# Kernel optimization log

Hardware: AMD Instinct MI355X
Metric: run time of the kernel (lower is better)

The kernel has to match this reference:

```python
import jax, jax.numpy as jnp
import numpy as np
from jax import lax

B, BANDS, H, W = 128, 100, 9, 9
S = 10  # BANDS = S*S spectral grid
C_HID, OUT_CH = 16, 10
K = 3  # 3x3x3x3 kernel, SAME padding
DN = ('NCEFGH', 'OIEFGH', 'NCEFGH')  # 4 spatial dims E,F,G,H


def _conv4d(x, w, b):
    # x: [B, Cin, S, S, H, W], w: [Cout, Cin, 3, 3, 3, 3]
    y = lax.conv_general_dilated(x, w, (1, 1, 1, 1), 'SAME', dimension_numbers=DN)
    return y + b[None, :, None, None, None, None]


def setup_inputs() -> dict:
    key = jax.random.key(0)
    ks = jax.random.split(key, 13)
    x = jax.random.normal(ks[0], (B, BANDS, H, W), dtype=jnp.float32)
    p = {}
    cin = 1
    for i in range(5):
        p[f'w{i+1}'] = jax.random.normal(ks[1 + 2 * i], (C_HID, cin, K, K, K, K), dtype=jnp.float32) * 0.1
        p[f'b{i+1}'] = jax.random.normal(ks[2 + 2 * i], (C_HID,), dtype=jnp.float32) * 0.1
        cin = C_HID
    p['fc_w'] = jax.random.normal(ks[11], (OUT_CH, C_HID), dtype=jnp.float32) * 0.1
    p['fc_b'] = jax.random.normal(ks[12], (OUT_CH,), dtype=jnp.float32) * 0.1
    return {'x': x, **p}


def reference(x, w1, b1, w2, b2, w3, b3, w4, b4, w5, b5, fc_w, fc_b):
    b, c, h, w = x.shape
    # center_pixel: spectral difference w.r.t. the center pixel
    ctr = x[:, :, h // 2, w // 2]                 # [B, bands]
    local = x - ctr[:, :, None, None]             # [B, bands, H, W]
    # compute_local_feature: fold spectral axis into a 2D grid -> 6D, 1 channel
    pt = local.reshape(b, 1, S, S, h, w)          # [B, 1, S, S, H, W]
    a = pt
    for wgt, bia in ((w1, b1), (w2, b2), (w3, b3), (w4, b4), (w5, b5)):
        a = jax.nn.relu(_conv4d(a, wgt, bia))
    # sideout2d: pool spectral dims, per-pixel MLP readout
    feat = a.mean(axis=(2, 3))                    # [B, 16, H, W]
    out = jnp.einsum('bchw,oc->bohw', feat, fc_w) + fc_b[None, :, None, None]
    return out
```

## Files before the change

kernel.cpp:

```cpp
#include <hip/hip_runtime.h>

#define BB 128
#define CH 16
#define NBANDS 100
#define OUTC 10

#define P1PLANE 121
#define P1POS   17424

#define PFPLANE 132
#define PFPOS   19008

#define LPLANE  4224
#define NPLANES 16
#define LDSTILE (NPLANES*LPLANE + 768)
#define NCHUNK  (NPLANES*132)
#define NKP     5
#define WPL4    (NKP*9*64)

typedef unsigned short ushort_t;
typedef unsigned int uint_t;
typedef __attribute__((ext_vector_type(8))) short short8;
typedef __attribute__((ext_vector_type(4))) float f32x4;

__device__ __forceinline__ ushort_t f2bf(float f) {
    unsigned u = __float_as_uint(f);
    unsigned r = u + 0x7fffu + ((u >> 16) & 1u);
    return (ushort_t)(r >> 16);
}
__device__ __forceinline__ uint_t pk2(float a, float b) {
    return (uint_t)f2bf(a) | ((uint_t)f2bf(b) << 16);
}
__device__ __forceinline__ int swz(int x) { return x ^ ((x >> 3) & 0x30); }

template<int CTRL>
__device__ __forceinline__ short8 dpp_shift(short8 v) {
    union { short8 s; int i[4]; } a, b;
    a.s = v;
    #pragma unroll
    for (int k = 0; k < 4; ++k)
        b.i[k] = __builtin_amdgcn_update_dpp(0, a.i[k], CTRL, 0xf, 0xf, true);
    return b.s;
}

__global__ void prep_kernel(const float* __restrict__ x, float* __restrict__ bufP, int nb) {
    int idx = blockIdx.x * 256 + threadIdx.x;
    if (idx >= nb * PFPOS) return;
    int pos = idx % PFPOS;
    int b = idx / PFPOS;
    int e = pos / 1584;
    int r = pos % 1584;
    int f = r / 132;
    int s = r % 132;
    int g = s / 12, h = s % 12;
    float v = 0.f;
    if (e >= 1 && e <= 10 && f >= 1 && f <= 10 && g >= 1 && g <= 9 && h >= 1 && h <= 9) {
        const float* xp = x + ((size_t)b * NBANDS + (e - 1) * 10 + (f - 1)) * 81;
        v = xp[(g - 1) * 9 + (h - 1)] - xp[40];
    }
    bufP[idx] = v;
}

__global__ void pack_w_kernel(const float* __restrict__ w2, const float* __restrict__ w3,
                              const float* __restrict__ w4, const float* __restrict__ w5,
                              uint4* __restrict__ wp) {
    int t = blockIdx.x * 256 + threadIdx.x;
    if (t >= WPL4) return;
    int layer = blockIdx.y;
    const float* w = (layer == 0) ? w2 : (layer == 1) ? w3 : (layer == 2) ? w4 : w5;
    int l = t & 63, pd = t >> 6;
    int kp = pd / 9, q = pd % 9;
    int co = l & 15, kh = l >> 4;
    int m = kh >> 1, cih = (kh & 1) * 8;
    int c = 2 * kp + m;
    uint_t r[4] = {0, 0, 0, 0};
    if (c <= 8) {
        int tap = c * 9 + q;
        #pragma unroll
        for (int jj = 0; jj < 4; ++jj) {
            ushort_t lo = f2bf(w[(co * 16 + cih + 2 * jj) * 81 + tap]);
            ushort_t hi = f2bf(w[(co * 16 + cih + 2 * jj + 1) * 81 + tap]);
            r[jj] = (uint_t)lo | ((uint_t)hi << 16);
        }
    }
    uint4 v; v.x = r[0]; v.y = r[1]; v.z = r[2]; v.w = r[3];
    wp[(size_t)layer * WPL4 + t] = v;
}

__global__ __launch_bounds__(256) void conv1_kernel(
    const float* __restrict__ in, const float* __restrict__ w,
    const float* __restrict__ bias, ushort_t* __restrict__ out) {
    int idx = blockIdx.x * 256 + threadIdx.x;
    if (idx >= 900) return;
    int b = blockIdx.z;
    int co0 = blockIdx.y * 8;
    int g = idx % 9;
    int f = (idx / 9) % 10;
    int e = idx / 90;

    float acc[8][9];
    #pragma unroll
    for (int co = 0; co < 8; ++co) {
        float bv = bias[co0 + co];
        #pragma unroll
        for (int h = 0; h < 9; ++h) acc[co][h] = bv;
    }

    const float* ip = in + (size_t)b * PFPOS;
    #pragma unroll
    for (int de = 0; de < 3; ++de)
    #pragma unroll
    for (int df = 0; df < 3; ++df)
    #pragma unroll
    for (int dg = 0; dg < 3; ++dg) {
        const float4* rp4 = (const float4*)(ip + ((e + de) * 12 + (f + df)) * PFPLANE + (g + dg) * 12);
        float4 r0 = rp4[0], r1 = rp4[1], r2 = rp4[2];
        float v[12] = {r0.x, r0.y, r0.z, r0.w, r1.x, r1.y, r1.z, r1.w, r2.x, r2.y, r2.z, r2.w};
        #pragma unroll
        for (int dh = 0; dh < 3; ++dh) {
            int tap = de * 27 + df * 9 + dg * 3 + dh;
            #pragma unroll
            for (int co = 0; co < 8; ++co) {
                float ws = w[(co0 + co) * 81 + tap];
                #pragma unroll
                for (int h = 0; h < 9; ++h)
                    acc[co][h] = fmaf(ws, v[h + dh], acc[co][h]);
            }
        }
    }

    ushort_t* op = out + ((size_t)b * P1POS + ((e + 1) * 12 + (f + 1)) * P1PLANE + (g + 1) * 11 + 1) * 16 + co0;
    #pragma unroll
    for (int h = 0; h < 9; ++h) {
        uint4 q;
        q.x = pk2(fmaxf(acc[0][h], 0.f), fmaxf(acc[1][h], 0.f));
        q.y = pk2(fmaxf(acc[2][h], 0.f), fmaxf(acc[3][h], 0.f));
        q.z = pk2(fmaxf(acc[4][h], 0.f), fmaxf(acc[5][h], 0.f));
        q.w = pk2(fmaxf(acc[6][h], 0.f), fmaxf(acc[7][h], 0.f));
        *(uint4*)(op + h * 16) = q;
    }
}

__device__ __forceinline__ void stage_chunk(const ushort_t* __restrict__ gin,
                                            char* __restrict__ sIn, int i, int eb, int fb) {
    int h = i % 12;
    int gp = i / 12;
    int g = gp % 11;
    int pl = gp / 11;
    int pe = pl >> 2, pf = pl & 3;
    int e2 = eb + pe, f2 = fb + pf;
    bool valid = (e2 >= 1) & (e2 <= 10) & (f2 >= 1) & (f2 <= 10) &
                 (g >= 1) & (g <= 9) & (h >= 1) & (h <= 9);
    uint4 q0 = make_uint4(0, 0, 0, 0), q1 = q0;
    if (valid) {
        const uint4* g4 = (const uint4*)(gin + (size_t)((e2 * 12 + f2) * P1PLANE + g * 11 + h) * 16);
        q0 = g4[0]; q1 = g4[1];
    }
    *(uint4*)(sIn + swz(i * 32))      = q0;
    *(uint4*)(sIn + swz(i * 32 + 16)) = q1;
}

template<int GO0, int NT, int GI0, int GI1>
__device__ __forceinline__ void conv_col(
    const char* __restrict__ sIn, const short8* __restrict__ wv8, int l, int we, int wf,
    float bv, int e_out, int f_out, ushort_t* __restrict__ gout) {

    int h = l & 15, kh = l >> 4;
    int m = kh >> 1;
    int half16 = (kh & 1) * 16;
    int co = l & 15;

    f32x4 acc[NT];
    #pragma unroll
    for (int t = 0; t < NT; ++t) acc[t] = f32x4{bv, bv, bv, bv};

    #pragma unroll 1
    for (int kp = 0; kp < NKP; ++kp) {
        int c = 2 * kp + m; if (c > 8) c = 8;
        int pl = (we + c / 3) * 4 + (wf + c % 3);
        int pbase = pl * LPLANE + h * 32 + half16;

        short8 Bf[9];
        #pragma unroll
        for (int q = 0; q < 9; ++q) Bf[q] = wv8[(kp * 9 + q) * 64 + l];

        #pragma unroll
        for (int gi = GI0; gi <= GI1; ++gi) {
            short8 a1 = *(const short8*)(sIn + swz(pbase + gi * 384));
            short8 a0 = dpp_shift<0x111>(a1);
            short8 a2 = dpp_shift<0x101>(a1);
            #pragma unroll
            for (int dg = 0; dg < 3; ++dg) {
                int go = gi + 1 - dg;
                if (go >= GO0 && go < GO0 + NT) {
                    int t = go - GO0;
                    acc[t] = __builtin_amdgcn_mfma_f32_16x16x32_bf16(a0, Bf[dg * 3 + 0], acc[t], 0, 0, 0);
                    acc[t] = __builtin_amdgcn_mfma_f32_16x16x32_bf16(a1, Bf[dg * 3 + 1], acc[t], 0, 0, 0);
                    acc[t] = __builtin_amdgcn_mfma_f32_16x16x32_bf16(a2, Bf[dg * 3 + 2], acc[t], 0, 0, 0);
                }
            }
        }
    }

    #pragma unroll
    for (int t = 0; t < NT; ++t) {
        int go = GO0 + t;
        int base = ((e_out * 12 + f_out) * P1PLANE + go * 11) * 16 + co;
        #pragma unroll
        for (int reg = 0; reg < 4; ++reg) {
            int rr = kh * 4 + reg;
            if (rr >= 1 && rr <= 9)
                gout[base + rr * 16] = f2bf(fmaxf(acc[t][reg], 0.f));
        }
    }
}

__global__ __launch_bounds__(512, 4) void conv_mfma_kernel(
    const ushort_t* __restrict__ in, const uint4* __restrict__ wp,
    const float* __restrict__ bias, ushort_t* __restrict__ out) {

    __shared__ __align__(16) char sIn[LDSTILE];

    int tid = threadIdx.x;
    int b  = blockIdx.y;
    int eb = (blockIdx.x / 5) * 2;
    int fb = (blockIdx.x % 5) * 2;

    const ushort_t* gin = in + (size_t)b * P1POS * 16;
    #pragma unroll
    for (int k = 0; k < 4; ++k)
        stage_chunk(gin, sIn, tid + k * 512, eb, fb);
    if (tid < 64)
        stage_chunk(gin, sIn, tid + 2048, eb, fb);
    __syncthreads();

    int l = tid & 63, wv = tid >> 6;
    int col = wv >> 1, gs = wv & 1;
    int we = col >> 1, wf = col & 1;
    int e_out = eb + 1 + we;
    int f_out = fb + 1 + wf;
    float bv = bias[l & 15];

    ushort_t* gout = out + (size_t)b * P1POS * 16;
    const short8* wv8 = (const short8*)wp;

    if (gs == 0)
        conv_col<1, 5, 0, 6>(sIn, wv8, l, we, wf, bv, e_out, f_out, gout);
    else
        conv_col<6, 4, 5, 10>(sIn, wv8, l, we, wf, bv, e_out, f_out, gout);
}

__global__ __launch_bounds__(704) void featfc_kernel(
    const ushort_t* __restrict__ a, const float* __restrict__ fcw,
    const float* __restrict__ fcb, float* __restrict__ out) {
    int t = threadIdx.x;
    if (t >= 648) return;
    int b = blockIdx.x;
    int j = t & 7;
    int gh = t >> 3;
    int g = gh / 9, h = gh % 9;
    const uint_t* base = (const uint_t*)(a + (size_t)b * P1POS * 16 +
                                         (size_t)((g + 1) * 11 + (h + 1)) * 16) + j;
    float s0 = 0.f, s1 = 0.f;
    #pragma unroll 2
    for (int e = 1; e <= 10; ++e) {
        #pragma unroll
        for (int f = 1; f <= 10; ++f) {
            uint_t u = base[(size_t)(e * 12 + f) * P1PLANE * 8];
            s0 += __uint_as_float(u << 16);
            s1 += __uint_as_float(u & 0xffff0000u);
        }
    }
    s0 *= 0.01f; s1 *= 0.01f;

    float po[OUTC];
    #pragma unroll
    for (int o = 0; o < OUTC; ++o)
        po[o] = fmaf(fcw[o * 16 + 2 * j], s0, fcw[o * 16 + 2 * j + 1] * s1);
    #pragma unroll
    for (int o = 0; o < OUTC; ++o) {
        po[o] += __shfl_xor(po[o], 1);
        po[o] += __shfl_xor(po[o], 2);
        po[o] += __shfl_xor(po[o], 4);
    }
    out[((size_t)b * OUTC + j) * 81 + gh] = po[j] + fcb[j];
    if (j < 2)
        out[((size_t)b * OUTC + j + 8) * 81 + gh] = po[j + 8] + fcb[j + 8];
}

extern "C" void kernel_launch(void* const* d_in, const int* in_sizes, int n_in,
                              void* d_out, int out_size, void* d_ws, size_t ws_size,
                              hipStream_t stream) {
    const float* x   = (const float*)d_in[0];
    const float* w1  = (const float*)d_in[1];
    const float* b1  = (const float*)d_in[2];
    const float* w2  = (const float*)d_in[3];
    const float* b2  = (const float*)d_in[4];
    const float* w3  = (const float*)d_in[5];
    const float* b3  = (const float*)d_in[6];
    const float* w4  = (const float*)d_in[7];
    const float* b4  = (const float*)d_in[8];
    const float* w5  = (const float*)d_in[9];
    const float* b5  = (const float*)d_in[10];
    const float* fcw = (const float*)d_in[11];
    const float* fcb = (const float*)d_in[12];
    float* outp = (float*)d_out;

    char* wsc = (char*)d_ws;
    uint4* wp_all = (uint4*)wsc;
    size_t off = 4ull * WPL4 * sizeof(uint4);

    const size_t perb_bytes = (size_t)PFPOS * 4 + 2ull * P1POS * 16 * 2;
    size_t avail = (ws_size > off) ? ws_size - off : 0;
    int nbmax = (int)(avail / perb_bytes);
    if (nbmax < 1) nbmax = 1;
    if (nbmax > BB) nbmax = BB;

    float* bufP = (float*)(wsc + off);       off += (size_t)nbmax * PFPOS * 4;
    ushort_t* bufA = (ushort_t*)(wsc + off); off += (size_t)nbmax * P1POS * 16 * 2;
    ushort_t* bufB = (ushort_t*)(wsc + off);

    dim3 pg((WPL4 + 255) / 256, 4);
    pack_w_kernel<<<pg, 256, 0, stream>>>(w2, w3, w4, w5, wp_all);

    for (int b0 = 0; b0 < BB; b0 += nbmax) {
        int nb = BB - b0;
        if (nb > nbmax) nb = nbmax;

        int pt = nb * PFPOS;
        prep_kernel<<<(pt + 255) / 256, 256, 0, stream>>>(x + (size_t)b0 * NBANDS * 81, bufP, nb);

        dim3 c1g(4, 2, nb);
        conv1_kernel<<<c1g, 256, 0, stream>>>(bufP, w1, b1, bufA);

        dim3 mg(25, nb);
        conv_mfma_kernel<<<mg, 512, 0, stream>>>(bufA, wp_all + 0 * WPL4, b2, bufB);
        conv_mfma_kernel<<<mg, 512, 0, stream>>>(bufB, wp_all + 1 * WPL4, b3, bufA);
        conv_mfma_kernel<<<mg, 512, 0, stream>>>(bufA, wp_all + 2 * WPL4, b4, bufB);
        conv_mfma_kernel<<<mg, 512, 0, stream>>>(bufB, wp_all + 3 * WPL4, b5, bufA);

        featfc_kernel<<<nb, 704, 0, stream>>>(bufA, fcw, fcb, outp + (size_t)b0 * OUTC * 81);
    }
}
```

Before: 418.0 us.

## Read conv activations directly from global memory instead of staging through LDS

The MFMA conv kernel no longer copies a halo tile into shared memory with a barrier. Each wave now loads its A fragments straight from the bf16 activation buffers and relies on the cache hierarchy for reuse. To replace the zero-fill the staging used to do, a new kernel zeroes the halo positions of both ping-pong buffers once, and extra workspace slack covers reads past the last plane. This drops the large LDS allocation and the sync, which should allow more resident blocks, at the cost of repeated global/L1 traffic for the overlapping taps.

```diff
diff --git a/kernel.cpp b/kernel.cpp
--- a/kernel.cpp
+++ b/kernel.cpp
@@ -11,10 +11,6 @@
 #define PFPLANE 132
 #define PFPOS   19008
 
-#define LPLANE  4224
-#define NPLANES 16
-#define LDSTILE (NPLANES*LPLANE + 768)
-#define NCHUNK  (NPLANES*132)
 #define NKP     5
 #define WPL4    (NKP*9*64)
 
@@ -31,7 +27,6 @@
 __device__ __forceinline__ uint_t pk2(float a, float b) {
     return (uint_t)f2bf(a) | ((uint_t)f2bf(b) << 16);
 }
-__device__ __forceinline__ int swz(int x) { return x ^ ((x >> 3) & 0x30); }
 
 template<int CTRL>
 __device__ __forceinline__ short8 dpp_shift(short8 v) {
@@ -59,6 +54,25 @@
         v = xp[(g - 1) * 9 + (h - 1)] - xp[40];
     }
     bufP[idx] = v;
+}
+
+__global__ void padzero_kernel(ushort_t* __restrict__ a, ushort_t* __restrict__ b, int nb) {
+    int idx = blockIdx.x * 256 + threadIdx.x;
+    if (idx >= nb * P1POS) return;
+    int pos = idx % P1POS;
+    int e = pos / 1452;
+    int r = pos % 1452;
+    int f = r / 121;
+    int s = r % 121;
+    int g = s / 11, h = s % 11;
+    bool pad = !(e >= 1 && e <= 10 && f >= 1 && f <= 10 && g >= 1 && g <= 9 && h >= 1 && h <= 9);
+    if (pad) {
+        uint4 z = make_uint4(0, 0, 0, 0);
+        *(uint4*)(a + (size_t)idx * 16)     = z;
+        *(uint4*)(a + (size_t)idx * 16 + 8) = z;
+        *(uint4*)(b + (size_t)idx * 16)     = z;
+        *(uint4*)(b + (size_t)idx * 16 + 8) = z;
+    }
 }
 
 __global__ void pack_w_kernel(const float* __restrict__ w2, const float* __restrict__ w3,
@@ -141,29 +155,10 @@
     }
 }
 
-__device__ __forceinline__ void stage_chunk(const ushort_t* __restrict__ gin,
-                                            char* __restrict__ sIn, int i, int eb, int fb) {
-    int h = i % 12;
-    int gp = i / 12;
-    int g = gp % 11;
-    int pl = gp / 11;
-    int pe = pl >> 2, pf = pl & 3;
-    int e2 = eb + pe, f2 = fb + pf;
-    bool valid = (e2 >= 1) & (e2 <= 10) & (f2 >= 1) & (f2 <= 10) &
-                 (g >= 1) & (g <= 9) & (h >= 1) & (h <= 9);
-    uint4 q0 = make_uint4(0, 0, 0, 0), q1 = q0;
-    if (valid) {
-        const uint4* g4 = (const uint4*)(gin + (size_t)((e2 * 12 + f2) * P1PLANE + g * 11 + h) * 16);
-        q0 = g4[0]; q1 = g4[1];
-    }
-    *(uint4*)(sIn + swz(i * 32))      = q0;
-    *(uint4*)(sIn + swz(i * 32 + 16)) = q1;
-}
-
 template<int GO0, int NT, int GI0, int GI1>
-__device__ __forceinline__ void conv_col(
-    const char* __restrict__ sIn, const short8* __restrict__ wv8, int l, int we, int wf,
-    float bv, int e_out, int f_out, ushort_t* __restrict__ gout) {
+__device__ __forceinline__ void conv_col_g(
+    const ushort_t* __restrict__ gin, const short8* __restrict__ wv8, int l, int we, int wf,
+    int eb, int fb, float bv, int e_out, int f_out, ushort_t* __restrict__ gout) {
 
     int h = l & 15, kh = l >> 4;
     int m = kh >> 1;
@@ -177,8 +172,9 @@
     #pragma unroll 1
     for (int kp = 0; kp < NKP; ++kp) {
         int c = 2 * kp + m; if (c > 8) c = 8;
-        int pl = (we + c / 3) * 4 + (wf + c % 3);
-        int pbase = pl * LPLANE + h * 32 + half16;
+        int e2 = eb + we + c / 3;
+        int f2 = fb + wf + c % 3;
+        const char* pbase = (const char*)gin + ((size_t)(e2 * 12 + f2) * P1PLANE) * 32 + h * 32 + half16;
 
         short8 Bf[9];
         #pragma unroll
@@ -186,7 +182,7 @@
 
         #pragma unroll
         for (int gi = GI0; gi <= GI1; ++gi) {
-            short8 a1 = *(const short8*)(sIn + swz(pbase + gi * 384));
+            short8 a1 = *(const short8*)(pbase + gi * (11 * 32));
             short8 a0 = dpp_shift<0x111>(a1);
             short8 a2 = dpp_shift<0x101>(a1);
             #pragma unroll
@@ -219,20 +215,12 @@
     const ushort_t* __restrict__ in, const uint4* __restrict__ wp,
     const float* __restrict__ bias, ushort_t* __restrict__ out) {
 
-    __shared__ __align__(16) char sIn[LDSTILE];
-
     int tid = threadIdx.x;
     int b  = blockIdx.y;
     int eb = (blockIdx.x / 5) * 2;
     int fb = (blockIdx.x % 5) * 2;
 
     const ushort_t* gin = in + (size_t)b * P1POS * 16;
-    #pragma unroll
-    for (int k = 0; k < 4; ++k)
-        stage_chunk(gin, sIn, tid + k * 512, eb, fb);
-    if (tid < 64)
-        stage_chunk(gin, sIn, tid + 2048, eb, fb);
-    __syncthreads();
 
     int l = tid & 63, wv = tid >> 6;
     int col = wv >> 1, gs = wv & 1;
@@ -245,9 +233,9 @@
     const short8* wv8 = (const short8*)wp;
 
     if (gs == 0)
-        conv_col<1, 5, 0, 6>(sIn, wv8, l, we, wf, bv, e_out, f_out, gout);
+        conv_col_g<1, 5, 0, 6>(gin, wv8, l, we, wf, eb, fb, bv, e_out, f_out, gout);
     else
-        conv_col<6, 4, 5, 10>(sIn, wv8, l, we, wf, bv, e_out, f_out, gout);
+        conv_col_g<6, 4, 5, 10>(gin, wv8, l, we, wf, eb, fb, bv, e_out, f_out, gout);
 }
 
 __global__ __launch_bounds__(704) void featfc_kernel(
@@ -311,7 +299,7 @@
     size_t off = 4ull * WPL4 * sizeof(uint4);
 
     const size_t perb_bytes = (size_t)PFPOS * 4 + 2ull * P1POS * 16 * 2;
-    size_t avail = (ws_size > off) ? ws_size - off : 0;
+    size_t avail = (ws_size > off + 8192) ? ws_size - off - 8192 : 0;
     int nbmax = (int)(avail / perb_bytes);
     if (nbmax < 1) nbmax = 1;
     if (nbmax > BB) nbmax = BB;
@@ -322,6 +310,9 @@
 
     dim3 pg((WPL4 + 255) / 256, 4);
     pack_w_kernel<<<pg, 256, 0, stream>>>(w2, w3, w4, w5, wp_all);
+
+    int pz = nbmax * P1POS;
+    padzero_kernel<<<(pz + 255) / 256, 256, 0, stream>>>(bufA, bufB, nbmax);
 
     for (int b0 = 0; b0 < BB; b0 += nbmax) {
         int nb = BB - b0;
```

Result: slower. 477.5 us (+14.2%).
